# Kernel optimization log

Measured on AMD Instinct MI355X. Metric: run time of the kernel, lower is better.

The kernel has to match this reference:

```python
import jax, jax.numpy as jnp
import numpy as np

BS, N_LINKS, MAX_LEN = 8192, 512, 32
D_LINK, D_PATH, D_READ, N_OUT = 32, 128, 256, 3
BN_EPS = 1e-5


def setup_inputs() -> dict:
    key = jax.random.key(0)
    ks = jax.random.split(key, 16)
    capa = jax.random.uniform(ks[0], (BS, N_LINKS), jnp.float32, 0.5, 1.0) * 100.0
    avail = jax.random.uniform(ks[1], (BS, N_LINKS), jnp.float32) * capa
    loss = jax.random.uniform(ks[2], (BS, N_LINKS), jnp.float32) * 0.05
    demand = jax.random.uniform(ks[3], (BS,), jnp.float32) * 10.0
    path = jax.random.randint(ks[4], (BS, MAX_LEN), 0, N_LINKS)
    hop_num = jax.random.randint(ks[5], (BS,), 1, MAX_LEN + 1)
    s = 0.1
    inp = {
        "demand": demand,
        "link_avail_capacity": avail,
        "link_capacity": capa,
        "link_loss": loss,
        "path": path,
        "hop_num": hop_num,
        # GRU params (PyTorch layout: [3H, D] gates ordered r,z,n)
        "gru_w_ih": jax.random.normal(ks[6], (3 * D_PATH, D_LINK), jnp.float32) * s,
        "gru_w_hh": jax.random.normal(ks[7], (3 * D_PATH, D_PATH), jnp.float32) * s,
        "gru_b_ih": jax.random.normal(ks[8], (3 * D_PATH,), jnp.float32) * s,
        "gru_b_hh": jax.random.normal(ks[9], (3 * D_PATH,), jnp.float32) * s,
        "bn_gamma": jnp.ones((D_PATH,), jnp.float32),
        "bn_beta": jnp.zeros((D_PATH,), jnp.float32),
        # stacked readout heads [N_OUT, ...]
        "rW1": jax.random.normal(ks[10], (N_OUT, D_PATH, D_READ), jnp.float32) * s,
        "rb1": jnp.zeros((N_OUT, D_READ), jnp.float32),
        "rW2": jax.random.normal(ks[11], (N_OUT, D_READ, D_READ), jnp.float32) * s,
        "rb2": jnp.zeros((N_OUT, D_READ), jnp.float32),
        "rW3": jax.random.normal(ks[12], (N_OUT, D_READ, 1), jnp.float32) * s,
        "rb3": jnp.zeros((N_OUT, 1), jnp.float32),
    }
    return inp


def _gru_scan(x_bt, h0, w_ih, w_hh, b_ih, b_hh):
    # x_bt: [B, T, D]; h0: [B, H] -> outputs [B, T, H]
    H = h0.shape[-1]
    def step(h, x_t):
        gi = x_t @ w_ih.T + b_ih          # [B, 3H]
        gh = h @ w_hh.T + b_hh            # [B, 3H]
        i_r, i_z, i_n = gi[:, :H], gi[:, H:2*H], gi[:, 2*H:]
        h_r, h_z, h_n = gh[:, :H], gh[:, H:2*H], gh[:, 2*H:]
        r = jax.nn.sigmoid(i_r + h_r)
        z = jax.nn.sigmoid(i_z + h_z)
        n = jnp.tanh(i_n + r * h_n)
        h_new = (1.0 - z) * n + z * h
        return h_new, h_new
    _, outs = jax.lax.scan(step, h0, jnp.swapaxes(x_bt, 0, 1))
    return jnp.swapaxes(outs, 0, 1)


def reference(demand, link_avail_capacity, link_capacity, link_loss, path, hop_num,
              gru_w_ih, gru_w_hh, gru_b_ih, gru_b_hh, bn_gamma, bn_beta,
              rW1, rb1, rW2, rb2, rW3, rb3):
    bs, n_links = link_capacity.shape
    max_len = path.shape[1]
    max_capa = jax.lax.stop_gradient(jnp.max(link_capacity))
    # link_state: [B, n_links, D_LINK]; first D_LINK-4 channels are zeros
    feats = jnp.stack([
        link_avail_capacity / max_capa,
        link_capacity / max_capa,
        link_avail_capacity / link_capacity,
        link_loss,
    ], axis=-1)
    link_state = jnp.concatenate(
        [jnp.zeros((bs, n_links, D_LINK - 4), feats.dtype), feats], axis=-1)
    link_state = jax.lax.stop_gradient(link_state)  # original detaches
    # initial hidden: zeros except last channel = demand/max_capa
    h0 = jnp.concatenate(
        [jnp.zeros((bs, D_PATH - 1), feats.dtype), (demand / max_capa)[:, None]], axis=-1)
    # fused gather of link states along each path, masked past hop_num
    gathered = jnp.take_along_axis(link_state, path[:, :, None], axis=1)  # [B, T, D]
    mask = (jnp.arange(max_len)[None, :] < hop_num[:, None])[:, :, None]
    link_inputs = gathered * mask.astype(gathered.dtype)
    outputs = _gru_scan(link_inputs, h0, gru_w_ih, gru_w_hh, gru_b_ih, gru_b_hh)
    # extract hidden state at last hop of each path
    idx = (hop_num - 1)[:, None, None]
    flow = jnp.take_along_axis(outputs, idx, axis=1)[:, 0, :]  # [B, H]
    # BatchNorm1d (training mode: batch statistics, biased variance)
    mean = jnp.mean(flow, axis=0)
    var = jnp.mean((flow - mean) ** 2, axis=0)
    flow = (flow - mean) * jax.lax.rsqrt(var + BN_EPS) * bn_gamma + bn_beta
    # readout heads: Linear -> SELU -> Linear -> SELU -> Linear
    h1 = jax.nn.selu(jnp.einsum('bh,uhr->ubr', flow, rW1) + rb1[:, None, :])
    h2 = jax.nn.selu(jnp.einsum('ubr,urs->ubs', h1, rW2) + rb2[:, None, :])
    y = jnp.einsum('ubs,uso->ubo', h2, rW3) + rb3[:, None, :]  # [U, B, 1]
    return jnp.transpose(y[:, :, 0], (1, 0))  # [B, U]
```

## Files before the change

kernel.cpp:

```cpp
#include <hip/hip_runtime.h>


#define BS 8192
#define NL 512
#define ML 32
#define DP 128
#define DR 256
#define NJOB 512
#define ST 172

#define OFF_SUM    64
#define OFF_SSQ    192
#define OFF_CUR    576
#define OFF_PERM   640
#define OFF_WHH16  (OFF_PERM + BS)
#define OFF_W1     (OFF_WHH16 + 24576)
#define OFF_W2     (OFF_W1 + 49152)
#define OFF_FEATS  (OFF_W2 + 98304)
#define OFF_FLOW   (OFF_FEATS + BS*ML*4)

#define FEATS_BLOCKS 1024
#define MAX_BLOCKS   256
#define WPREP_BLOCKS 1344
#define SORT_BID     (FEATS_BLOCKS + MAX_BLOCKS + WPREP_BLOCKS)
#define PREP_GRID    (SORT_BID + 1)

typedef _Float16 f16x8 __attribute__((ext_vector_type(8)));
typedef float    f32x4 __attribute__((ext_vector_type(4)));

__device__ __forceinline__ float sigmoidf_(float x){ return 1.0f/(1.0f+__expf(-x)); }
__device__ __forceinline__ float tanhf_(float x){
  float t = __expf(-2.0f*fabsf(x));
  float r = (1.0f-t)/(1.0f+t);
  return copysignf(r, x);
}
__device__ __forceinline__ float seluf_(float x){
  const float sc = 1.0507009873554805f, al = 1.6732632423543772f;
  return x > 0.0f ? sc*x : sc*al*(__expf(x)-1.0f);
}

__global__ void prep_all(const int* __restrict__ path, const int* __restrict__ hop,
                         const float* __restrict__ avail, const float* __restrict__ capa,
                         const float* __restrict__ loss, const float* __restrict__ whh,
                         const float* __restrict__ rW1, const float* __restrict__ rW2,
                         float* ws){
  const int bid = blockIdx.x;
  const int tid = threadIdx.x;

  if (bid < FEATS_BLOCKS){
    int idx = bid*256 + tid;
    int b = idx >> 5, t = idx & 31;
    float4 f = make_float4(0.f, 0.f, 0.f, 0.f);
    if (t < hop[b]){
      int l = path[idx];
      float a = avail[b*NL + l];
      float c = capa [b*NL + l];
      f.x = a; f.y = c; f.z = a / c; f.w = loss[b*NL + l];
    }
    ((float4*)(ws + OFF_FEATS))[idx] = f;
  } else if (bid < FEATS_BLOCKS + MAX_BLOCKS){
    const float4* c4 = (const float4*)capa;
    const int n4 = BS*NL/4;
    float m = 0.0f;
    for (int i = (bid - FEATS_BLOCKS)*256 + tid; i < n4; i += MAX_BLOCKS*256){
      float4 v = c4[i];
      m = fmaxf(m, fmaxf(fmaxf(v.x, v.y), fmaxf(v.z, v.w)));
    }
    #pragma unroll
    for (int o = 32; o > 0; o >>= 1) m = fmaxf(m, __shfl_down(m, o, 64));
    if ((tid & 63) == 0) atomicMax((int*)ws, __float_as_int(m));
  } else if (bid < SORT_BID){
    _Float16* whh16 = (_Float16*)(ws + OFF_WHH16);
    _Float16* w1    = (_Float16*)(ws + OFF_W1);
    _Float16* w2    = (_Float16*)(ws + OFF_W2);
    int i = (bid - FEATS_BLOCKS - MAX_BLOCKS)*256 + tid;
    if (i < 49152){
      whh16[i] = (_Float16)whh[i];
    } else if (i < 147456){
      int j = i - 49152; int u = j >> 15; int rem = j & 32767; int n = rem >> 7; int k = rem & 127;
      w1[j] = (_Float16)rW1[u*32768 + k*256 + n];
    } else if (i < 344064){
      int j = i - 147456; int u = j >> 16; int rem = j & 65535; int n = rem >> 8; int k = rem & 255;
      w2[j] = (_Float16)rW2[u*65536 + k*256 + n];
    }
  } else {
    __shared__ int hist[32], start[32];
    for (int i = 64 + tid; i < 640; i += 256) ws[i] = 0.0f;
    if (tid < 32) hist[tid] = 0;
    __syncthreads();
    for (int b = tid; b < BS; b += 256) atomicAdd(&hist[32 - hop[b]], 1);
    __syncthreads();
    if (tid == 0){ int acc = 0; for (int i = 0; i < 32; ++i){ start[i] = acc; acc += hist[i]; } }
    __syncthreads();
    int* perm = (int*)ws + OFF_PERM;
    for (int b = tid; b < BS; b += 256){
      int pos = atomicAdd(&start[32 - hop[b]], 1);
      perm[pos] = b;
    }
  }
}

__launch_bounds__(512, 4)
__global__ void kgru(const float* __restrict__ demand, const int* __restrict__ hop,
                     const float* __restrict__ wih, const float* __restrict__ bih,
                     const float* __restrict__ bhh, float* __restrict__ ws,
                     float* __restrict__ flow){
  __shared__ _Float16 hHI[2][16*ST];
  __shared__ _Float16 hLO[2][16*ST];
  const int tid  = threadIdx.x;
  const int w    = tid >> 6;
  const int lane = tid & 63;
  const int lm   = lane & 15;
  const int qd   = lane >> 4;
  const int ch   = w*16 + lm;
  const float inv_maxc = 1.0f / ws[0];
  const int* perm = (const int*)ws + OFF_PERM;
  const float* feats = ws + OFF_FEATS;
  const _Float16* whh16 = (const _Float16*)(ws + OFF_WHH16);

  const int bid = blockIdx.x;
  const int q = (bid < 256) ? bid : 767 - bid;

  for (int idx = tid; idx < 1024; idx += 512){
    const int buf = idx >> 9;
    const int rem = idx & 511;
    const int m   = rem >> 5;
    const int c   = 128 + (rem & 31);
    hHI[buf][m*ST + c] = (_Float16)0.f;
    hLO[buf][m*ST + c] = (_Float16)0.f;
  }

  f16x8 bfr[5], bfz[5], bfnh[4], bfni;
  #pragma unroll
  for (int kc = 0; kc < 4; ++kc){
    bfr[kc]  = *(const f16x8*)(whh16 + (      ch)*128 + kc*32 + qd*8);
    bfz[kc]  = *(const f16x8*)(whh16 + (128 + ch)*128 + kc*32 + qd*8);
    bfnh[kc] = *(const f16x8*)(whh16 + (256 + ch)*128 + kc*32 + qd*8);
  }
  bfr[4] = (f16x8)0; bfz[4] = (f16x8)0; bfni = (f16x8)0;
  if (qd == 0){
    #pragma unroll
    for (int j = 0; j < 4; ++j){
      float s = (j < 2) ? inv_maxc : 1.0f;
      bfr[4][j] = (_Float16)(wih[(      ch)*32 + 28 + j] * s);
      bfz[4][j] = (_Float16)(wih[(128 + ch)*32 + 28 + j] * s);
      bfni[j]   = (_Float16)(wih[(256 + ch)*32 + 28 + j] * s);
    }
  }
  const float bR  = bih[ch]     + bhh[ch];
  const float bZ  = bih[128+ch] + bhh[128+ch];
  const float bNI = bih[256+ch];
  const float bNH = bhh[256+ch];

  int it[4], hp[4];
  #pragma unroll
  for (int r = 0; r < 4; ++r){
    it[r] = perm[q*16 + qd*4 + r];
    hp[r] = hop[it[r]];
  }
  int tmax = max(max(hp[0],hp[1]), max(hp[2],hp[3]));
  tmax = max(tmax, __shfl_xor(tmax, 16, 64));
  tmax = max(tmax, __shfl_xor(tmax, 32, 64));

  const int fw_i = w*2 + (lane >> 2);
  const int fw_c = lane & 3;
  const bool fw  = (lane < 8);
  const int  fw_b = fw ? perm[q*16 + fw_i] : 0;

  __syncthreads();

  float hprev[4];
  #pragma unroll
  for (int r = 0; r < 4; ++r){
    float h0 = (ch == 127) ? demand[it[r]] * inv_maxc : 0.0f;
    hprev[r] = h0;
    const int m = qd*4 + r;
    _Float16 hi = (_Float16)h0;
    hHI[0][m*ST + ch] = hi;
    hLO[0][m*ST + ch] = (_Float16)(h0 - (float)hi);
  }
  if (fw){
    float v = feats[(fw_b*ML + 0)*4 + fw_c];
    _Float16 hi = (_Float16)v;
    hHI[0][fw_i*ST + 128 + fw_c] = hi;
    hLO[0][fw_i*ST + 128 + fw_c] = (_Float16)(v - (float)hi);
  }
  __syncthreads();

  for (int t = 0; t < tmax; ++t){
    const int cur = t & 1, nxt = cur ^ 1;
    if (fw && (t+1) < ML){
      float v = feats[(fw_b*ML + t + 1)*4 + fw_c];
      _Float16 hi = (_Float16)v;
      hHI[nxt][fw_i*ST + 128 + fw_c] = hi;
      hLO[nxt][fw_i*ST + 128 + fw_c] = (_Float16)(v - (float)hi);
    }

    f32x4 accr = {0.f,0.f,0.f,0.f}, accz = {0.f,0.f,0.f,0.f};
    f32x4 accnh = {0.f,0.f,0.f,0.f}, accni = {0.f,0.f,0.f,0.f};
    #pragma unroll
    for (int kc = 0; kc < 5; ++kc){
      const int off = lm*ST + kc*32 + qd*8;
      f16x8 ahi = *(const f16x8*)(&hHI[cur][off]);
      f16x8 alo = *(const f16x8*)(&hLO[cur][off]);
      accr = __builtin_amdgcn_mfma_f32_16x16x32_f16(ahi, bfr[kc], accr, 0, 0, 0);
      accr = __builtin_amdgcn_mfma_f32_16x16x32_f16(alo, bfr[kc], accr, 0, 0, 0);
      accz = __builtin_amdgcn_mfma_f32_16x16x32_f16(ahi, bfz[kc], accz, 0, 0, 0);
      accz = __builtin_amdgcn_mfma_f32_16x16x32_f16(alo, bfz[kc], accz, 0, 0, 0);
      if (kc < 4){
        accnh = __builtin_amdgcn_mfma_f32_16x16x32_f16(ahi, bfnh[kc], accnh, 0, 0, 0);
        accnh = __builtin_amdgcn_mfma_f32_16x16x32_f16(alo, bfnh[kc], accnh, 0, 0, 0);
      } else {
        accni = __builtin_amdgcn_mfma_f32_16x16x32_f16(ahi, bfni, accni, 0, 0, 0);
        accni = __builtin_amdgcn_mfma_f32_16x16x32_f16(alo, bfni, accni, 0, 0, 0);
      }
    }

    #pragma unroll
    for (int r = 0; r < 4; ++r){
      float rr = sigmoidf_(accr[r] + bR);
      float zz = sigmoidf_(accz[r] + bZ);
      float nn = tanhf_(accni[r] + bNI + rr*(accnh[r] + bNH));
      float hn = fmaf(zz, hprev[r] - nn, nn);
      if (t < hp[r]) hprev[r] = hn;
      const int m = qd*4 + r;
      _Float16 hi = (_Float16)hprev[r];
      hHI[nxt][m*ST + ch] = hi;
      hLO[nxt][m*ST + ch] = (_Float16)(hprev[r] - (float)hi);
    }
    __syncthreads();
  }

  float ssum = 0.f, ssq = 0.f;
  #pragma unroll
  for (int r = 0; r < 4; ++r){
    float v = hprev[r];
    flow[it[r]*DP + ch] = v;
    ssum += v;
    ssq  = fmaf(v, v, ssq);
  }
  ssum += __shfl_xor(ssum, 16, 64);  ssum += __shfl_xor(ssum, 32, 64);
  ssq  += __shfl_xor(ssq,  16, 64);  ssq  += __shfl_xor(ssq,  32, 64);
  if (qd == 0){
    atomicAdd(&ws[OFF_SUM + ch], ssum);
    atomicAdd(&ws[OFF_SSQ + ch], ssq);
  }
}

__launch_bounds__(256, 4)
__global__ void kmlp(const float* __restrict__ flow, const float* __restrict__ ws,
                     const float* __restrict__ gamma, const float* __restrict__ beta,
                     const float* __restrict__ rb1, const float* __restrict__ rb2,
                     const float* __restrict__ rW3, const float* __restrict__ rb3,
                     float* __restrict__ out){
  __shared__ _Float16 x_lds[32*136];
  __shared__ _Float16 h1_lds[32*264];
  __shared__ float aa[DP], bb[DP];
  __shared__ float y_part[4][32];
  const int tid  = threadIdx.x;
  const int w    = tid >> 6;
  const int lane = tid & 63;
  const int lm   = lane & 15;
  const int qd   = lane >> 4;
  const int b0   = blockIdx.x * 32;
  const int u    = blockIdx.y;
  const _Float16* w1 = (const _Float16*)(ws + OFF_W1) + u*(DR*DP);
  const _Float16* w2 = (const _Float16*)(ws + OFF_W2) + u*(DR*DR);

  if (tid < DP){
    float m = ws[OFF_SUM + tid] * (1.0f/BS);
    float q = ws[OFF_SSQ + tid] * (1.0f/BS);
    float rstd = rsqrtf(q - m*m + 1e-5f);
    float a = rstd * gamma[tid];
    aa[tid] = a;
    bb[tid] = fmaf(-m, a, beta[tid]);
  }
  __syncthreads();

  for (int idx = tid; idx < 32*DP; idx += 256){
    int i = idx >> 7, h = idx & 127;
    x_lds[i*136 + h] = (_Float16)fmaf(flow[(b0 + i)*DP + h], aa[h], bb[h]);
  }
  __syncthreads();

  for (int nt = 0; nt < 4; ++nt){
    const int n = (4*w + nt)*16 + lm;
    const float bias1 = rb1[u*DR + n];
    f16x8 b1[4];
    #pragma unroll
    for (int kc = 0; kc < 4; ++kc)
      b1[kc] = *(const f16x8*)(w1 + n*DP + kc*32 + qd*8);
    #pragma unroll
    for (int mt = 0; mt < 2; ++mt){
      f32x4 acc = {bias1, bias1, bias1, bias1};
      #pragma unroll
      for (int kc = 0; kc < 4; ++kc){
        f16x8 a1 = *(const f16x8*)(&x_lds[(mt*16 + lm)*136 + kc*32 + qd*8]);
        acc = __builtin_amdgcn_mfma_f32_16x16x32_f16(a1, b1[kc], acc, 0, 0, 0);
      }
      #pragma unroll
      for (int r = 0; r < 4; ++r)
        h1_lds[(mt*16 + qd*4 + r)*264 + n] = (_Float16)seluf_(acc[r]);
    }
  }
  __syncthreads();

  {
    float p[2][4] = {{0.f,0.f,0.f,0.f},{0.f,0.f,0.f,0.f}};
    for (int nt = 0; nt < 4; ++nt){
      const int n = (4*w + nt)*16 + lm;
      const float bias2 = rb2[u*DR + n];
      const float w3l   = rW3[u*DR + n];
      f16x8 b2[8];
      #pragma unroll
      for (int kc = 0; kc < 8; ++kc)
        b2[kc] = *(const f16x8*)(w2 + n*DR + kc*32 + qd*8);
      #pragma unroll
      for (int mt = 0; mt < 2; ++mt){
        f32x4 acc = {bias2, bias2, bias2, bias2};
        #pragma unroll
        for (int kc = 0; kc < 8; ++kc){
          f16x8 a2 = *(const f16x8*)(&h1_lds[(mt*16 + lm)*264 + kc*32 + qd*8]);
          acc = __builtin_amdgcn_mfma_f32_16x16x32_f16(a2, b2[kc], acc, 0, 0, 0);
        }
        #pragma unroll
        for (int r = 0; r < 4; ++r)
          p[mt][r] += seluf_(acc[r]) * w3l;
      }
    }
    #pragma unroll
    for (int mt = 0; mt < 2; ++mt){
      #pragma unroll
      for (int r = 0; r < 4; ++r){
        float v = p[mt][r];
        v += __shfl_xor(v, 1, 64);
        v += __shfl_xor(v, 2, 64);
        v += __shfl_xor(v, 4, 64);
        v += __shfl_xor(v, 8, 64);
        if (lm == 0) y_part[w][mt*16 + qd*4 + r] = v;
      }
    }
  }
  __syncthreads();
  if (tid < 32){
    float y = y_part[0][tid] + y_part[1][tid] + y_part[2][tid] + y_part[3][tid] + rb3[u];
    out[(b0 + tid)*3 + u] = y;
  }
}

extern "C" void kernel_launch(void* const* d_in, const int* in_sizes, int n_in,
                              void* d_out, int out_size, void* d_ws, size_t ws_size,
                              hipStream_t stream){
  const float* demand = (const float*)d_in[0];
  const float* avail  = (const float*)d_in[1];
  const float* capa   = (const float*)d_in[2];
  const float* loss   = (const float*)d_in[3];
  const int*   path   = (const int*)d_in[4];
  const int*   hop    = (const int*)d_in[5];
  const float* wih    = (const float*)d_in[6];
  const float* whh    = (const float*)d_in[7];
  const float* bih    = (const float*)d_in[8];
  const float* bhh    = (const float*)d_in[9];
  const float* gamma  = (const float*)d_in[10];
  const float* beta   = (const float*)d_in[11];
  const float* rW1    = (const float*)d_in[12];
  const float* rb1    = (const float*)d_in[13];
  const float* rW2    = (const float*)d_in[14];
  const float* rb2    = (const float*)d_in[15];
  const float* rW3    = (const float*)d_in[16];
  const float* rb3    = (const float*)d_in[17];
  float* ws  = (float*)d_ws;
  float* out = (float*)d_out;

  prep_all <<<PREP_GRID, 256, 0, stream>>>(path, hop, avail, capa, loss,
                                           whh, rW1, rW2, ws);
  kgru     <<<NJOB, 512, 0, stream>>>(demand, hop, wih, bih, bhh, ws, ws + OFF_FLOW);
  kmlp     <<<dim3(BS/32, 3), 256, 0, stream>>>(ws + OFF_FLOW, ws, gamma, beta,
                                                rb1, rb2, rW3, rb3, out);
}
```

Before: 225.7 us.

## Fuse prep, GRU and MLP into one persistent kernel with grid barriers

Replaces the three-kernel pipeline (prep, GRU, MLP) with a tiny init kernel plus a single 512-block kernel that uses software grid barriers between phases. The global hop-length sort becomes per-block histograms followed by a prefix scan, and the readout MLP runs on each block's GRU outputs still in registers and LDS, so the flow tensor never goes to global memory. This removes launch gaps and a global round trip, at the cost of three spin-wait grid barriers that need all 512 blocks co-resident and that give up after a timeout. The MLP tiling also changes to 16-row tiles covering all three heads per block.

```diff
diff --git a/kernel.cpp b/kernel.cpp
--- a/kernel.cpp
+++ b/kernel.cpp
@@ -11,19 +11,13 @@
 
 #define OFF_SUM    64
 #define OFF_SSQ    192
-#define OFF_CUR    576
+#define OFF_BAR    576
 #define OFF_PERM   640
-#define OFF_WHH16  (OFF_PERM + BS)
+#define OFF_BH     (OFF_PERM + BS)
+#define OFF_WHH16  (OFF_BH + 16384)
 #define OFF_W1     (OFF_WHH16 + 24576)
 #define OFF_W2     (OFF_W1 + 49152)
 #define OFF_FEATS  (OFF_W2 + 98304)
-#define OFF_FLOW   (OFF_FEATS + BS*ML*4)
-
-#define FEATS_BLOCKS 1024
-#define MAX_BLOCKS   256
-#define WPREP_BLOCKS 1344
-#define SORT_BID     (FEATS_BLOCKS + MAX_BLOCKS + WPREP_BLOCKS)
-#define PREP_GRID    (SORT_BID + 1)
 
 typedef _Float16 f16x8 __attribute__((ext_vector_type(8)));
 typedef float    f32x4 __attribute__((ext_vector_type(4)));
@@ -39,95 +33,143 @@
   return x > 0.0f ? sc*x : sc*al*(__expf(x)-1.0f);
 }
 
-__global__ void prep_all(const int* __restrict__ path, const int* __restrict__ hop,
-                         const float* __restrict__ avail, const float* __restrict__ capa,
-                         const float* __restrict__ loss, const float* __restrict__ whh,
-                         const float* __restrict__ rW1, const float* __restrict__ rW2,
-                         float* ws){
-  const int bid = blockIdx.x;
-  const int tid = threadIdx.x;
-
-  if (bid < FEATS_BLOCKS){
-    int idx = bid*256 + tid;
-    int b = idx >> 5, t = idx & 31;
-    float4 f = make_float4(0.f, 0.f, 0.f, 0.f);
-    if (t < hop[b]){
-      int l = path[idx];
-      float a = avail[b*NL + l];
-      float c = capa [b*NL + l];
-      f.x = a; f.y = c; f.z = a / c; f.w = loss[b*NL + l];
-    }
-    ((float4*)(ws + OFF_FEATS))[idx] = f;
-  } else if (bid < FEATS_BLOCKS + MAX_BLOCKS){
-    const float4* c4 = (const float4*)capa;
-    const int n4 = BS*NL/4;
-    float m = 0.0f;
-    for (int i = (bid - FEATS_BLOCKS)*256 + tid; i < n4; i += MAX_BLOCKS*256){
-      float4 v = c4[i];
-      m = fmaxf(m, fmaxf(fmaxf(v.x, v.y), fmaxf(v.z, v.w)));
-    }
-    #pragma unroll
-    for (int o = 32; o > 0; o >>= 1) m = fmaxf(m, __shfl_down(m, o, 64));
-    if ((tid & 63) == 0) atomicMax((int*)ws, __float_as_int(m));
-  } else if (bid < SORT_BID){
-    _Float16* whh16 = (_Float16*)(ws + OFF_WHH16);
-    _Float16* w1    = (_Float16*)(ws + OFF_W1);
-    _Float16* w2    = (_Float16*)(ws + OFF_W2);
-    int i = (bid - FEATS_BLOCKS - MAX_BLOCKS)*256 + tid;
-    if (i < 49152){
-      whh16[i] = (_Float16)whh[i];
-    } else if (i < 147456){
-      int j = i - 49152; int u = j >> 15; int rem = j & 32767; int n = rem >> 7; int k = rem & 127;
-      w1[j] = (_Float16)rW1[u*32768 + k*256 + n];
-    } else if (i < 344064){
-      int j = i - 147456; int u = j >> 16; int rem = j & 65535; int n = rem >> 8; int k = rem & 255;
-      w2[j] = (_Float16)rW2[u*65536 + k*256 + n];
-    }
-  } else {
-    __shared__ int hist[32], start[32];
-    for (int i = 64 + tid; i < 640; i += 256) ws[i] = 0.0f;
-    if (tid < 32) hist[tid] = 0;
-    __syncthreads();
-    for (int b = tid; b < BS; b += 256) atomicAdd(&hist[32 - hop[b]], 1);
-    __syncthreads();
-    if (tid == 0){ int acc = 0; for (int i = 0; i < 32; ++i){ start[i] = acc; acc += hist[i]; } }
-    __syncthreads();
-    int* perm = (int*)ws + OFF_PERM;
-    for (int b = tid; b < BS; b += 256){
-      int pos = atomicAdd(&start[32 - hop[b]], 1);
-      perm[pos] = b;
-    }
-  }
-}
+__device__ __forceinline__ void gbar(int* cnt){
+  __syncthreads();
+  if (threadIdx.x == 0){
+    __threadfence();
+    atomicAdd(cnt, 1);
+    long long t0 = clock64();
+    while (__hip_atomic_load(cnt, __ATOMIC_RELAXED, __HIP_MEMORY_SCOPE_AGENT) < NJOB){
+      __builtin_amdgcn_s_sleep(16);
+      if (clock64() - t0 > 50000000LL) break;
+    }
+    __threadfence();
+  }
+  __syncthreads();
+}
+
+__global__ void kinit(float* ws){
+  ws[threadIdx.x] = 0.0f;
+}
+
+struct P0 { int hist[32]; int off[32]; };
+struct P1 { _Float16 hHI[2][16*ST]; _Float16 hLO[2][16*ST]; };
+struct P2 { _Float16 x[16*136]; _Float16 h1[16*776];
+            float aa[DP]; float bb[DP]; float yacc[48]; };
+union SMem { P0 p0; P1 p1; P2 p2; };
 
 __launch_bounds__(512, 4)
-__global__ void kgru(const float* __restrict__ demand, const int* __restrict__ hop,
-                     const float* __restrict__ wih, const float* __restrict__ bih,
-                     const float* __restrict__ bhh, float* __restrict__ ws,
-                     float* __restrict__ flow){
-  __shared__ _Float16 hHI[2][16*ST];
-  __shared__ _Float16 hLO[2][16*ST];
+__global__ void fused(const float* __restrict__ demand, const int* __restrict__ hop,
+                      const int* __restrict__ path, const float* __restrict__ avail,
+                      const float* __restrict__ capa, const float* __restrict__ loss,
+                      const float* __restrict__ whh, const float* __restrict__ wih,
+                      const float* __restrict__ bih, const float* __restrict__ bhh,
+                      const float* __restrict__ gamma, const float* __restrict__ beta,
+                      const float* __restrict__ rW1, const float* __restrict__ rb1,
+                      const float* __restrict__ rW2, const float* __restrict__ rb2,
+                      const float* __restrict__ rW3, const float* __restrict__ rb3,
+                      float* ws, float* __restrict__ out){
+  __shared__ SMem sm;
+  int* bar = (int*)ws + OFF_BAR;
+  const int bid  = blockIdx.x;
   const int tid  = threadIdx.x;
+  const int gid  = bid*512 + tid;
   const int w    = tid >> 6;
   const int lane = tid & 63;
   const int lm   = lane & 15;
   const int qd   = lane >> 4;
   const int ch   = w*16 + lm;
+
+  {
+    const float4* c4 = (const float4*)capa;
+    float m = 0.0f;
+    #pragma unroll
+    for (int i = gid; i < BS*NL/4; i += 512*512){
+      float4 v = c4[i];
+      m = fmaxf(m, fmaxf(fmaxf(v.x, v.y), fmaxf(v.z, v.w)));
+    }
+    #pragma unroll
+    for (int o = 32; o > 0; o >>= 1) m = fmaxf(m, __shfl_down(m, o, 64));
+    if (lane == 0) atomicMax((int*)ws, __float_as_int(m));
+  }
+
+  {
+    _Float16* whh16 = (_Float16*)(ws + OFF_WHH16);
+    _Float16* w1t   = (_Float16*)(ws + OFF_W1);
+    _Float16* w2t   = (_Float16*)(ws + OFF_W2);
+    if (gid < 49152) whh16[gid] = (_Float16)whh[gid];
+    for (int i = gid; i < 294912; i += 262144){
+      if (i < 98304){
+        int u = i >> 15, rem = i & 32767, n = rem >> 7, k = rem & 127;
+        w1t[i] = (_Float16)rW1[u*32768 + k*256 + n];
+      } else {
+        int j = i - 98304;
+        int u = j >> 16, rem = j & 65535, n = rem >> 8, k = rem & 255;
+        w2t[j] = (_Float16)rW2[u*65536 + k*256 + n];
+      }
+    }
+  }
+
+  {
+    int b = gid >> 5, t = gid & 31;
+    float4 f = make_float4(0.f, 0.f, 0.f, 0.f);
+    if (t < hop[b]){
+      int l = path[gid];
+      float a = avail[b*NL + l];
+      float c = capa [b*NL + l];
+      f.x = a; f.y = c; f.z = a / c; f.w = loss[b*NL + l];
+    }
+    ((float4*)(ws + OFF_FEATS))[gid] = f;
+  }
+
+  {
+    if (tid < 32) sm.p0.hist[tid] = 0;
+    __syncthreads();
+    if (tid < 16) atomicAdd(&sm.p0.hist[32 - hop[bid*16 + tid]], 1);
+    __syncthreads();
+    if (tid < 32) ((int*)ws + OFF_BH)[bid*32 + tid] = sm.p0.hist[tid];
+  }
+
+  gbar(&bar[0]);
+
+  {
+    if (tid < 32){
+      const int* bh = (const int*)ws + OFF_BH;
+      int off = 0, tot = 0;
+      for (int b2 = 0; b2 < 512; ++b2){
+        int c = bh[b2*32 + tid];
+        tot += c;
+        if (b2 < bid) off += c;
+      }
+      int g = tot;
+      #pragma unroll
+      for (int o = 1; o < 32; o <<= 1){ int v = __shfl_up(g, o, 64); if (tid >= o) g += v; }
+      sm.p0.off[tid] = (g - tot) + off;
+    }
+    __syncthreads();
+    if (tid < 16){
+      int b = bid*16 + tid;
+      int k = 32 - hop[b];
+      int rank = 0;
+      for (int j = 0; j < 16; ++j)
+        rank += ((32 - hop[bid*16 + j]) == k && j < tid) ? 1 : 0;
+      ((int*)ws + OFF_PERM)[sm.p0.off[k] + rank] = b;
+    }
+  }
+
+  gbar(&bar[1]);
+
   const float inv_maxc = 1.0f / ws[0];
   const int* perm = (const int*)ws + OFF_PERM;
   const float* feats = ws + OFF_FEATS;
   const _Float16* whh16 = (const _Float16*)(ws + OFF_WHH16);
-
-  const int bid = blockIdx.x;
   const int q = (bid < 256) ? bid : 767 - bid;
 
   for (int idx = tid; idx < 1024; idx += 512){
-    const int buf = idx >> 9;
-    const int rem = idx & 511;
-    const int m   = rem >> 5;
-    const int c   = 128 + (rem & 31);
-    hHI[buf][m*ST + c] = (_Float16)0.f;
-    hLO[buf][m*ST + c] = (_Float16)0.f;
+    const int buf = idx >> 9, rem = idx & 511;
+    const int m = rem >> 5, c = 128 + (rem & 31);
+    sm.p1.hHI[buf][m*ST + c] = (_Float16)0.f;
+    sm.p1.hLO[buf][m*ST + c] = (_Float16)0.f;
   }
 
   f16x8 bfr[5], bfz[5], bfnh[4], bfni;
@@ -162,9 +204,9 @@
   tmax = max(tmax, __shfl_xor(tmax, 16, 64));
   tmax = max(tmax, __shfl_xor(tmax, 32, 64));
 
-  const int fw_i = w*2 + (lane >> 2);
-  const int fw_c = lane & 3;
-  const bool fw  = (lane < 8);
+  const int  fw_i = w*2 + (lane >> 2);
+  const int  fw_c = lane & 3;
+  const bool fw   = (lane < 8);
   const int  fw_b = fw ? perm[q*16 + fw_i] : 0;
 
   __syncthreads();
@@ -176,14 +218,14 @@
     hprev[r] = h0;
     const int m = qd*4 + r;
     _Float16 hi = (_Float16)h0;
-    hHI[0][m*ST + ch] = hi;
-    hLO[0][m*ST + ch] = (_Float16)(h0 - (float)hi);
+    sm.p1.hHI[0][m*ST + ch] = hi;
+    sm.p1.hLO[0][m*ST + ch] = (_Float16)(h0 - (float)hi);
   }
   if (fw){
     float v = feats[(fw_b*ML + 0)*4 + fw_c];
     _Float16 hi = (_Float16)v;
-    hHI[0][fw_i*ST + 128 + fw_c] = hi;
-    hLO[0][fw_i*ST + 128 + fw_c] = (_Float16)(v - (float)hi);
+    sm.p1.hHI[0][fw_i*ST + 128 + fw_c] = hi;
+    sm.p1.hLO[0][fw_i*ST + 128 + fw_c] = (_Float16)(v - (float)hi);
   }
   __syncthreads();
 
@@ -192,8 +234,8 @@
     if (fw && (t+1) < ML){
       float v = feats[(fw_b*ML + t + 1)*4 + fw_c];
       _Float16 hi = (_Float16)v;
-      hHI[nxt][fw_i*ST + 128 + fw_c] = hi;
-      hLO[nxt][fw_i*ST + 128 + fw_c] = (_Float16)(v - (float)hi);
+      sm.p1.hHI[nxt][fw_i*ST + 128 + fw_c] = hi;
+      sm.p1.hLO[nxt][fw_i*ST + 128 + fw_c] = (_Float16)(v - (float)hi);
     }
 
     f32x4 accr = {0.f,0.f,0.f,0.f}, accz = {0.f,0.f,0.f,0.f};
@@ -201,8 +243,8 @@
     #pragma unroll
     for (int kc = 0; kc < 5; ++kc){
       const int off = lm*ST + kc*32 + qd*8;
-      f16x8 ahi = *(const f16x8*)(&hHI[cur][off]);
-      f16x8 alo = *(const f16x8*)(&hLO[cur][off]);
+      f16x8 ahi = *(const f16x8*)(&sm.p1.hHI[cur][off]);
+      f16x8 alo = *(const f16x8*)(&sm.p1.hLO[cur][off]);
       accr = __builtin_amdgcn_mfma_f32_16x16x32_f16(ahi, bfr[kc], accr, 0, 0, 0);
       accr = __builtin_amdgcn_mfma_f32_16x16x32_f16(alo, bfr[kc], accr, 0, 0, 0);
       accz = __builtin_amdgcn_mfma_f32_16x16x32_f16(ahi, bfz[kc], accz, 0, 0, 0);
@@ -225,126 +267,103 @@
       if (t < hp[r]) hprev[r] = hn;
       const int m = qd*4 + r;
       _Float16 hi = (_Float16)hprev[r];
-      hHI[nxt][m*ST + ch] = hi;
-      hLO[nxt][m*ST + ch] = (_Float16)(hprev[r] - (float)hi);
+      sm.p1.hHI[nxt][m*ST + ch] = hi;
+      sm.p1.hLO[nxt][m*ST + ch] = (_Float16)(hprev[r] - (float)hi);
     }
     __syncthreads();
   }
 
-  float ssum = 0.f, ssq = 0.f;
+  {
+    float ssum = 0.f, ssq = 0.f;
+    #pragma unroll
+    for (int r = 0; r < 4; ++r){ ssum += hprev[r]; ssq = fmaf(hprev[r], hprev[r], ssq); }
+    ssum += __shfl_xor(ssum, 16, 64);  ssum += __shfl_xor(ssum, 32, 64);
+    ssq  += __shfl_xor(ssq,  16, 64);  ssq  += __shfl_xor(ssq,  32, 64);
+    if (qd == 0){
+      atomicAdd(&ws[OFF_SUM + ch], ssum);
+      atomicAdd(&ws[OFF_SSQ + ch], ssq);
+    }
+  }
+
+  gbar(&bar[2]);
+
+  if (tid < DP){
+    float m  = ws[OFF_SUM + tid] * (1.0f/BS);
+    float qq = ws[OFF_SSQ + tid] * (1.0f/BS);
+    float rstd = rsqrtf(qq - m*m + 1e-5f);
+    float a = rstd * gamma[tid];
+    sm.p2.aa[tid] = a;
+    sm.p2.bb[tid] = fmaf(-m, a, beta[tid]);
+  }
+  if (tid < 48) sm.p2.yacc[tid] = 0.f;
+  __syncthreads();
+
   #pragma unroll
-  for (int r = 0; r < 4; ++r){
-    float v = hprev[r];
-    flow[it[r]*DP + ch] = v;
-    ssum += v;
-    ssq  = fmaf(v, v, ssq);
-  }
-  ssum += __shfl_xor(ssum, 16, 64);  ssum += __shfl_xor(ssum, 32, 64);
-  ssq  += __shfl_xor(ssq,  16, 64);  ssq  += __shfl_xor(ssq,  32, 64);
-  if (qd == 0){
-    atomicAdd(&ws[OFF_SUM + ch], ssum);
-    atomicAdd(&ws[OFF_SSQ + ch], ssq);
-  }
-}
-
-__launch_bounds__(256, 4)
-__global__ void kmlp(const float* __restrict__ flow, const float* __restrict__ ws,
-                     const float* __restrict__ gamma, const float* __restrict__ beta,
-                     const float* __restrict__ rb1, const float* __restrict__ rb2,
-                     const float* __restrict__ rW3, const float* __restrict__ rb3,
-                     float* __restrict__ out){
-  __shared__ _Float16 x_lds[32*136];
-  __shared__ _Float16 h1_lds[32*264];
-  __shared__ float aa[DP], bb[DP];
-  __shared__ float y_part[4][32];
-  const int tid  = threadIdx.x;
-  const int w    = tid >> 6;
-  const int lane = tid & 63;
-  const int lm   = lane & 15;
-  const int qd   = lane >> 4;
-  const int b0   = blockIdx.x * 32;
-  const int u    = blockIdx.y;
-  const _Float16* w1 = (const _Float16*)(ws + OFF_W1) + u*(DR*DP);
-  const _Float16* w2 = (const _Float16*)(ws + OFF_W2) + u*(DR*DR);
-
-  if (tid < DP){
-    float m = ws[OFF_SUM + tid] * (1.0f/BS);
-    float q = ws[OFF_SSQ + tid] * (1.0f/BS);
-    float rstd = rsqrtf(q - m*m + 1e-5f);
-    float a = rstd * gamma[tid];
-    aa[tid] = a;
-    bb[tid] = fmaf(-m, a, beta[tid]);
-  }
-  __syncthreads();
-
-  for (int idx = tid; idx < 32*DP; idx += 256){
-    int i = idx >> 7, h = idx & 127;
-    x_lds[i*136 + h] = (_Float16)fmaf(flow[(b0 + i)*DP + h], aa[h], bb[h]);
-  }
-  __syncthreads();
-
-  for (int nt = 0; nt < 4; ++nt){
-    const int n = (4*w + nt)*16 + lm;
-    const float bias1 = rb1[u*DR + n];
-    f16x8 b1[4];
+  for (int r = 0; r < 4; ++r)
+    sm.p2.x[(qd*4 + r)*136 + ch] =
+      (_Float16)fmaf(hprev[r], sm.p2.aa[ch], sm.p2.bb[ch]);
+  __syncthreads();
+
+  {
+    const _Float16* w1t = (const _Float16*)(ws + OFF_W1);
+    f16x8 a1[4];
     #pragma unroll
     for (int kc = 0; kc < 4; ++kc)
-      b1[kc] = *(const f16x8*)(w1 + n*DP + kc*32 + qd*8);
-    #pragma unroll
-    for (int mt = 0; mt < 2; ++mt){
-      f32x4 acc = {bias1, bias1, bias1, bias1};
-      #pragma unroll
-      for (int kc = 0; kc < 4; ++kc){
-        f16x8 a1 = *(const f16x8*)(&x_lds[(mt*16 + lm)*136 + kc*32 + qd*8]);
-        acc = __builtin_amdgcn_mfma_f32_16x16x32_f16(a1, b1[kc], acc, 0, 0, 0);
-      }
+      a1[kc] = *(const f16x8*)(&sm.p2.x[lm*136 + kc*32 + qd*8]);
+    #pragma unroll
+    for (int ti = 0; ti < 6; ++ti){
+      const int nt = w + ti*8;
+      const int u  = nt >> 4;
+      const int nl = ((nt & 15) << 4) + lm;
+      const float b1v = rb1[u*DR + nl];
+      f16x8 bf1[4];
+      #pragma unroll
+      for (int kc = 0; kc < 4; ++kc)
+        bf1[kc] = *(const f16x8*)(w1t + u*32768 + nl*128 + kc*32 + qd*8);
+      f32x4 acc = {b1v, b1v, b1v, b1v};
+      #pragma unroll
+      for (int kc = 0; kc < 4; ++kc)
+        acc = __builtin_amdgcn_mfma_f32_16x16x32_f16(a1[kc], bf1[kc], acc, 0, 0, 0);
       #pragma unroll
       for (int r = 0; r < 4; ++r)
-        h1_lds[(mt*16 + qd*4 + r)*264 + n] = (_Float16)seluf_(acc[r]);
-    }
-  }
-  __syncthreads();
-
-  {
-    float p[2][4] = {{0.f,0.f,0.f,0.f},{0.f,0.f,0.f,0.f}};
-    for (int nt = 0; nt < 4; ++nt){
-      const int n = (4*w + nt)*16 + lm;
-      const float bias2 = rb2[u*DR + n];
-      const float w3l   = rW3[u*DR + n];
-      f16x8 b2[8];
-      #pragma unroll
-      for (int kc = 0; kc < 8; ++kc)
-        b2[kc] = *(const f16x8*)(w2 + n*DR + kc*32 + qd*8);
-      #pragma unroll
-      for (int mt = 0; mt < 2; ++mt){
-        f32x4 acc = {bias2, bias2, bias2, bias2};
-        #pragma unroll
-        for (int kc = 0; kc < 8; ++kc){
-          f16x8 a2 = *(const f16x8*)(&h1_lds[(mt*16 + lm)*264 + kc*32 + qd*8]);
-          acc = __builtin_amdgcn_mfma_f32_16x16x32_f16(a2, b2[kc], acc, 0, 0, 0);
-        }
-        #pragma unroll
-        for (int r = 0; r < 4; ++r)
-          p[mt][r] += seluf_(acc[r]) * w3l;
-      }
-    }
-    #pragma unroll
-    for (int mt = 0; mt < 2; ++mt){
+        sm.p2.h1[(qd*4 + r)*776 + nt*16 + lm] = (_Float16)seluf_(acc[r]);
+    }
+  }
+  __syncthreads();
+
+  {
+    const _Float16* w2t = (const _Float16*)(ws + OFF_W2);
+    #pragma unroll
+    for (int ti = 0; ti < 6; ++ti){
+      const int nt = w + ti*8;
+      const int u  = nt >> 4;
+      const int nl = ((nt & 15) << 4) + lm;
+      const float b2v = rb2[u*DR + nl];
+      const float w3v = rW3[u*DR + nl];
+      f32x4 acc = {b2v, b2v, b2v, b2v};
+      #pragma unroll
+      for (int kc = 0; kc < 8; ++kc){
+        f16x8 a2  = *(const f16x8*)(&sm.p2.h1[lm*776 + u*256 + kc*32 + qd*8]);
+        f16x8 bf2 = *(const f16x8*)(w2t + u*65536 + nl*256 + kc*32 + qd*8);
+        acc = __builtin_amdgcn_mfma_f32_16x16x32_f16(a2, bf2, acc, 0, 0, 0);
+      }
       #pragma unroll
       for (int r = 0; r < 4; ++r){
-        float v = p[mt][r];
+        float v = seluf_(acc[r]) * w3v;
         v += __shfl_xor(v, 1, 64);
         v += __shfl_xor(v, 2, 64);
         v += __shfl_xor(v, 4, 64);
         v += __shfl_xor(v, 8, 64);
-        if (lm == 0) y_part[w][mt*16 + qd*4 + r] = v;
-      }
-    }
-  }
-  __syncthreads();
-  if (tid < 32){
-    float y = y_part[0][tid] + y_part[1][tid] + y_part[2][tid] + y_part[3][tid] + rb3[u];
-    out[(b0 + tid)*3 + u] = y;
+        if (lm == 0) atomicAdd(&sm.p2.yacc[u*16 + qd*4 + r], v);
+      }
+    }
+  }
+  __syncthreads();
+
+  if (tid < 48){
+    const int u = tid >> 4, m = tid & 15;
+    const int item = ((const int*)ws + OFF_PERM)[q*16 + m];
+    out[item*3 + u] = sm.p2.yacc[tid] + rb3[u];
   }
 }
 
@@ -372,9 +391,8 @@
   float* ws  = (float*)d_ws;
   float* out = (float*)d_out;
 
-  prep_all <<<PREP_GRID, 256, 0, stream>>>(path, hop, avail, capa, loss,
-                                           whh, rW1, rW2, ws);
-  kgru     <<<NJOB, 512, 0, stream>>>(demand, hop, wih, bih, bhh, ws, ws + OFF_FLOW);
-  kmlp     <<<dim3(BS/32, 3), 256, 0, stream>>>(ws + OFF_FLOW, ws, gamma, beta,
-                                                rb1, rb2, rW3, rb3, out);
-}
+  kinit <<<1, 640, 0, stream>>>(ws);
+  fused <<<NJOB, 512, 0, stream>>>(demand, hop, path, avail, capa, loss,
+                                   whh, wih, bih, bhh, gamma, beta,
+                                   rW1, rb1, rW2, rb2, rW3, rb3, ws, out);
+}
```

After: 396.9 us. 75.9% more time.
